# Performance work log

Measured on AMD Instinct MI355X. Metric: run time of the kernel, lower is better.

## Reference

```python
import jax, jax.numpy as jnp
import numpy as np

DIM = 512
HEADS = 16
HEAD_DIM = DIM // HEADS
SCALE = HEAD_DIM ** -0.5


def setup_inputs() -> dict:
    key = jax.random.key(0)
    k = jax.random.split(key, 6)
    B_, N = 2048, 49
    nW = 64
    x = jax.random.normal(k[0], (B_, N, DIM), dtype=jnp.float32)
    mask = jax.random.normal(k[1], (nW, N, N), dtype=jnp.float32)
    W_qkv = jax.random.normal(k[2], (3 * DIM, DIM), dtype=jnp.float32) * 0.02
    b_qkv = jnp.zeros((3 * DIM,), dtype=jnp.float32)
    W_proj = jax.random.normal(k[3], (DIM, DIM), dtype=jnp.float32) * 0.02
    b_proj = jnp.zeros((DIM,), dtype=jnp.float32)
    return {"x": x, "mask": mask, "W_qkv": W_qkv, "b_qkv": b_qkv,
            "W_proj": W_proj, "b_proj": b_proj}


def reference(x, mask, W_qkv, b_qkv, W_proj, b_proj):
    B_, N, C = x.shape
    H, d = HEADS, HEAD_DIM
    nW = mask.shape[0]
    # qkv projection: [B_, N, 3, H, d] -> q,k,v each [B_, H, N, d]
    qkv = (x @ W_qkv.T + b_qkv).reshape(B_, N, 3, H, d)
    qkv = jnp.transpose(qkv, (2, 0, 3, 1, 4))
    q, k, v = qkv[0], qkv[1], qkv[2]
    attn = jnp.einsum('bhnd,bhmd->bhnm', q * SCALE, k)  # [B_, H, N, N]
    # add per-window additive mask, broadcast over B_//nW groups and heads
    attn = attn.reshape(B_ // nW, nW, H, N, N) + mask[None, :, None, :, :]
    attn = attn.reshape(B_, H, N, N)
    attn = jax.nn.softmax(attn, axis=-1)
    out = jnp.einsum('bhnm,bhmd->bhnd', attn, v)  # [B_, H, N, d]
    out = jnp.transpose(out, (0, 2, 1, 3)).reshape(B_, N, C)
    return out @ W_proj.T + b_proj
```

## Files before the change

kernel.cpp:

```cpp
#include <hip/hip_runtime.h>


typedef unsigned short ushort_t;
typedef __bf16 bf16x8 __attribute__((ext_vector_type(8)));
typedef float f32x4 __attribute__((ext_vector_type(4)));
typedef unsigned short us8 __attribute__((ext_vector_type(8)));

#define SCALE_F 0.17677669529663687f

__device__ __forceinline__ ushort_t f2bf(float f) {
  unsigned u = __builtin_bit_cast(unsigned, f);
  u += 0x7FFFu + ((u >> 16) & 1u);
  return (ushort_t)(u >> 16);
}

__device__ __forceinline__ void gload_lds16(const void* g, void* l) {
  __builtin_amdgcn_global_load_lds(
      (const __attribute__((address_space(1))) void*)g,
      (__attribute__((address_space(3))) void*)l, 16, 0, 0);
}

__global__ __launch_bounds__(256) void k_cvt(const float* __restrict__ in,
                                             ushort_t* __restrict__ out, int n4) {
  int i = blockIdx.x * blockDim.x + threadIdx.x;
  if (i >= n4) return;
  float4 v = reinterpret_cast<const float4*>(in)[i];
  ushort4 o = make_ushort4(f2bf(v.x), f2bf(v.y), f2bf(v.z), f2bf(v.w));
  reinterpret_cast<ushort4*>(out)[i] = o;
}

__global__ __launch_bounds__(256) void k_gemm1f(const float* __restrict__ X,
                                                const ushort_t* __restrict__ W,
                                                const float* __restrict__ bias,
                                                ushort_t* __restrict__ out_qkv) {
  __shared__ __align__(16) float    Asf[128][64];
  __shared__ __align__(16) ushort_t Ws[128][64];
  constexpr int nt_o = 12;

  const int tid  = threadIdx.x;
  const int lane = tid & 63;
  const int wv   = tid >> 6;
  const int wr   = wv >> 1, wc = wv & 1;

  const int cpx = gridDim.x >> 3;
  const int lid = (blockIdx.x & 7) * cpx + (blockIdx.x >> 3);
  const int bm  = lid / nt_o;
  const int bo  = lid - bm * nt_o;
  const size_t m0 = (size_t)bm * 128;
  const int o0    = bo * 128;

  f32x4 acc[4][4];
#pragma unroll
  for (int i = 0; i < 4; i++)
#pragma unroll
    for (int j = 0; j < 4; j++) acc[i][j] = f32x4{0.f, 0.f, 0.f, 0.f};

  const int l15 = lane & 15;
  const int lq  = lane >> 4;
  int schA[4];
#pragma unroll
  for (int i = 0; i < 4; i++)
    schA[i] = (l15 ^ ((i * 4 + lq) & 15)) * 4;

  const int srowW = wv * 32 + (lane >> 3);
  const int schW  = ((lane & 7) ^ (lane >> 3)) * 8;
  const ushort_t* Wg = W + (size_t)(o0 + srowW) * 512 + schW;

  for (int kt = 0; kt < 8; ++kt) {
    const int k0 = kt * 64;
#pragma unroll
    for (int i = 0; i < 8; i++) {
      const float* g = X + (m0 + wv * 32 + i * 4 + lq) * 512 + k0 + schA[i & 3];
      gload_lds16(g, &Asf[wv * 32 + i * 4][0]);
    }
#pragma unroll
    for (int i = 0; i < 4; i++)
      gload_lds16(Wg + (size_t)i * (8 * 512) + k0, &Ws[wv * 32 + i * 8][0]);
    __syncthreads();

    const int fr = lane & 15;
#pragma unroll
    for (int kk = 0; kk < 2; ++kk) {
      const int cbW = (((kk * 4 + lq) ^ (lane & 7)) << 3);
      uint4 br[4];
#pragma unroll
      for (int ni = 0; ni < 4; ni++)
        br[ni] = *reinterpret_cast<const uint4*>(&Ws[wc * 64 + ni * 16 + fr][cbW]);
      bf16x8 ar[4];
      const int L0 = kk * 8 + lq * 2;
      const int s0 = (L0 ^ fr) * 4;
      const int s1 = ((L0 + 1) ^ fr) * 4;
#pragma unroll
      for (int mi = 0; mi < 4; mi++) {
        const float4 fa = *reinterpret_cast<const float4*>(&Asf[wr * 64 + mi * 16 + fr][s0]);
        const float4 fb = *reinterpret_cast<const float4*>(&Asf[wr * 64 + mi * 16 + fr][s1]);
        bf16x8 t;
        t[0] = (__bf16)fa.x; t[1] = (__bf16)fa.y; t[2] = (__bf16)fa.z; t[3] = (__bf16)fa.w;
        t[4] = (__bf16)fb.x; t[5] = (__bf16)fb.y; t[6] = (__bf16)fb.z; t[7] = (__bf16)fb.w;
        ar[mi] = t;
      }
#pragma unroll
      for (int mi = 0; mi < 4; mi++)
#pragma unroll
        for (int ni = 0; ni < 4; ni++)
          acc[mi][ni] = __builtin_amdgcn_mfma_f32_16x16x32_bf16(
              ar[mi], __builtin_bit_cast(bf16x8, br[ni]), acc[mi][ni], 0, 0, 0);
    }
    __syncthreads();
  }

  const int colbase = lane & 15;
  const int rowgrp  = (lane >> 4) * 4;
#pragma unroll
  for (int mi = 0; mi < 4; mi++) {
#pragma unroll
    for (int r = 0; r < 4; r++) {
      const size_t t = m0 + wr * 64 + mi * 16 + rowgrp + r;
      ushort_t* rowp = out_qkv + t * 1536;
#pragma unroll
      for (int ni = 0; ni < 4; ni++) {
        const int o = o0 + wc * 64 + ni * 16 + colbase;
        rowp[o] = f2bf(acc[mi][ni][r] + bias[o]);
      }
    }
  }
}

__global__ __launch_bounds__(256) void k_gemmB(const ushort_t* __restrict__ A,
                                               const ushort_t* __restrict__ W,
                                               const float* __restrict__ bias,
                                               float* __restrict__ out_f,
                                               int nt_o) {
  __shared__ __align__(16) ushort_t As[128][64];
  __shared__ __align__(16) ushort_t Ws[128][64];

  const int tid  = threadIdx.x;
  const int lane = tid & 63;
  const int wv   = tid >> 6;
  const int wr   = wv >> 1, wc = wv & 1;

  const int cpx = gridDim.x >> 3;
  const int lid = (blockIdx.x & 7) * cpx + (blockIdx.x >> 3);
  const int bm  = lid / nt_o;
  const int bo  = lid - bm * nt_o;
  const size_t m0 = (size_t)bm * 128;
  const int o0    = bo * 128;

  f32x4 acc[4][4];
#pragma unroll
  for (int i = 0; i < 4; i++)
#pragma unroll
    for (int j = 0; j < 4; j++) acc[i][j] = f32x4{0.f, 0.f, 0.f, 0.f};

  const int srow   = wv * 32 + (lane >> 3);
  const int schunk = (((lane & 7) ^ (lane >> 3)) * 8);

  for (int kt = 0; kt < 8; ++kt) {
    const int k0 = kt * 64;
#pragma unroll
    for (int i = 0; i < 4; i++)
      gload_lds16(A + (m0 + srow + i * 8) * 512 + k0 + schunk,
                  &As[wv * 32 + i * 8][0]);
#pragma unroll
    for (int i = 0; i < 4; i++)
      gload_lds16(W + (size_t)(o0 + srow + i * 8) * 512 + k0 + schunk,
                  &Ws[wv * 32 + i * 8][0]);
    __syncthreads();
    const int fr = lane & 15;
#pragma unroll
    for (int kk = 0; kk < 2; ++kk) {
      const int ch = kk * 4 + (lane >> 4);
      const int cb = ((ch ^ (lane & 7)) << 3);
      uint4 ar[4], br[4];
#pragma unroll
      for (int mi = 0; mi < 4; mi++)
        ar[mi] = *reinterpret_cast<const uint4*>(&As[wr * 64 + mi * 16 + fr][cb]);
#pragma unroll
      for (int ni = 0; ni < 4; ni++)
        br[ni] = *reinterpret_cast<const uint4*>(&Ws[wc * 64 + ni * 16 + fr][cb]);
#pragma unroll
      for (int mi = 0; mi < 4; mi++)
#pragma unroll
        for (int ni = 0; ni < 4; ni++)
          acc[mi][ni] = __builtin_amdgcn_mfma_f32_16x16x32_bf16(
              __builtin_bit_cast(bf16x8, ar[mi]),
              __builtin_bit_cast(bf16x8, br[ni]), acc[mi][ni], 0, 0, 0);
    }
    __syncthreads();
  }

  const int colbase = lane & 15;
  const int rowgrp  = (lane >> 4) * 4;
#pragma unroll
  for (int ni = 0; ni < 4; ni++) {
    const int o = o0 + wc * 64 + ni * 16 + colbase;
    const float bv = bias[o];
#pragma unroll
    for (int mi = 0; mi < 4; mi++) {
      const size_t mrow = m0 + wr * 64 + mi * 16 + rowgrp;
#pragma unroll
      for (int r = 0; r < 4; r++)
        out_f[(mrow + r) * 512 + o] = acc[mi][ni][r] + bv;
    }
  }
}

__global__ __launch_bounds__(256) void k_attn4(const ushort_t* __restrict__ qkv,
                                               const float* __restrict__ mask,
                                               ushort_t* __restrict__ aout) {
  __shared__ __align__(16) ushort_t Vt[4][32][64];
  __shared__ __align__(16) ushort_t Ps[4][64][64];

  const int tid  = threadIdx.x;
  const int lane = tid & 63;
  const int wv   = tid >> 6;
  const int blk  = blockIdx.x;
  const int b    = blk >> 2;
  const int h    = (blk & 3) * 4 + wv;
  const int w    = b & 63;
  const size_t tb = (size_t)b * 49 * 1536 + (size_t)h * 32;
  const ushort_t* qb = qkv + tb;
  const ushort_t* kb = qkv + tb + 512;
  const ushort_t* vb = qkv + tb + 1024;

  {
    uint4* vz = reinterpret_cast<uint4*>(&Vt[wv][0][0]);
#pragma unroll
    for (int i = 0; i < 4; i++) vz[i * 64 + lane] = make_uint4(0, 0, 0, 0);
  }
  __syncthreads();
#pragma unroll
  for (int i = 0; i < 4; i++) {
    const int e = lane + (i << 6);
    if (e < 196) {
      const int n = e >> 2, d0 = (e & 3) * 8;
      uint4 raw = *reinterpret_cast<const uint4*>(vb + (size_t)n * 1536 + d0);
      us8 ev = __builtin_bit_cast(us8, raw);
#pragma unroll
      for (int j = 0; j < 8; j++)
        Vt[wv][d0 + j][(((n >> 3) ^ j) << 3) | (n & 7)] = ev[j];
    }
  }

  const int arow = lane & 15;
  const int kc   = (lane >> 4) * 8;
  const int rg   = (lane >> 4) * 4;

  uint4 kf[4];
#pragma unroll
  for (int ni = 0; ni < 4; ni++)
    kf[ni] = *reinterpret_cast<const uint4*>(kb + (size_t)(ni * 16 + arow) * 1536 + kc);

  float rsum[4][4];

#pragma unroll
  for (int hm = 0; hm < 2; hm++) {
    f32x4 s2[2][4];
#pragma unroll
    for (int j = 0; j < 2; j++) {
      const int mt = hm * 2 + j;
      uint4 qraw = *reinterpret_cast<const uint4*>(qb + (size_t)(mt * 16 + arow) * 1536 + kc);
      bf16x8 qa = __builtin_bit_cast(bf16x8, qraw);
#pragma unroll
      for (int ni = 0; ni < 4; ni++) {
        f32x4 z = {0.f, 0.f, 0.f, 0.f};
        s2[j][ni] = __builtin_amdgcn_mfma_f32_16x16x32_bf16(
            qa, __builtin_bit_cast(bf16x8, kf[ni]), z, 0, 0, 0);
      }
    }
#pragma unroll
    for (int j = 0; j < 2; j++) {
      const int mt = hm * 2 + j;
#pragma unroll
      for (int r = 0; r < 4; r++) {
        const int qr = mt * 16 + rg + r;
        float sv[4];
        float mx = -1e30f;
#pragma unroll
        for (int ni = 0; ni < 4; ni++) {
          const int col = ni * 16 + arow;
          float v;
          if (qr < 49 && col < 49)
            v = s2[j][ni][r] * SCALE_F + mask[(size_t)w * 2401 + qr * 49 + col];
          else
            v = -1e30f;
          sv[ni] = v;
          mx = fmaxf(mx, v);
        }
#pragma unroll
        for (int off = 1; off < 16; off <<= 1) mx = fmaxf(mx, __shfl_xor(mx, off));
        float sum = 0.f;
        const int prow = rg + r;
#pragma unroll
        for (int ni = 0; ni < 4; ni++) {
          float p = __expf(sv[ni] - mx);
          sum += p;
          const int pcol = ni * 16 + arow;
          Ps[wv][mt * 16 + prow]
            [(((pcol >> 3) ^ (prow & 7)) << 3) | (pcol & 7)] = f2bf(p);
        }
#pragma unroll
        for (int off = 1; off < 16; off <<= 1) sum += __shfl_xor(sum, off);
        rsum[mt][r] = sum;
      }
    }
  }

  __syncthreads();

  uint4 vf0[2], vf1[2];
#pragma unroll
  for (int kk = 0; kk < 2; kk++) {
    const int ch = kk * 4 + (lane >> 4);
    const int cb = ((ch ^ (lane & 7)) << 3);
    vf0[kk] = *reinterpret_cast<const uint4*>(&Vt[wv][arow][cb]);
    vf1[kk] = *reinterpret_cast<const uint4*>(&Vt[wv][16 + arow][cb]);
  }

#pragma unroll
  for (int mt = 0; mt < 4; mt++) {
    f32x4 o0 = {0.f, 0.f, 0.f, 0.f}, o1 = {0.f, 0.f, 0.f, 0.f};
#pragma unroll
    for (int kk = 0; kk < 2; kk++) {
      const int ch = kk * 4 + (lane >> 4);
      const int cb = ((ch ^ (lane & 7)) << 3);
      uint4 praw = *reinterpret_cast<const uint4*>(&Ps[wv][mt * 16 + arow][cb]);
      bf16x8 pa = __builtin_bit_cast(bf16x8, praw);
      o0 = __builtin_amdgcn_mfma_f32_16x16x32_bf16(
          pa, __builtin_bit_cast(bf16x8, vf0[kk]), o0, 0, 0, 0);
      o1 = __builtin_amdgcn_mfma_f32_16x16x32_bf16(
          pa, __builtin_bit_cast(bf16x8, vf1[kk]), o1, 0, 0, 0);
    }
#pragma unroll
    for (int r = 0; r < 4; r++) {
      const int qr = mt * 16 + rg + r;
      if (qr < 49) {
        const float inv = 1.f / rsum[mt][r];
        aout[((size_t)b * 49 + qr) * 512 + h * 32 + arow]      = f2bf(o0[r] * inv);
        aout[((size_t)b * 49 + qr) * 512 + h * 32 + 16 + arow] = f2bf(o1[r] * inv);
      }
    }
  }
}

extern "C" void kernel_launch(void* const* d_in, const int* in_sizes, int n_in,
                              void* d_out, int out_size, void* d_ws, size_t ws_size,
                              hipStream_t stream) {
  const float* x      = (const float*)d_in[0];
  const float* mask   = (const float*)d_in[1];
  const float* W_qkv  = (const float*)d_in[2];
  const float* b_qkv  = (const float*)d_in[3];
  const float* W_proj = (const float*)d_in[4];
  const float* b_proj = (const float*)d_in[5];
  float* out = (float*)d_out;

  ushort_t* ws     = (ushort_t*)d_ws;
  ushort_t* qkvb   = ws;
  ushort_t* aoutb  = ws + 154140672UL;
  ushort_t* wqkvb  = ws + 205520896UL;
  ushort_t* wprojb = ws + 206307328UL;

  const int n4q = 786432 / 4, n4p = 262144 / 4;
  k_cvt<<<(n4q + 255) / 256, 256, 0, stream>>>(W_qkv, wqkvb, n4q);
  k_cvt<<<(n4p + 255) / 256, 256, 0, stream>>>(W_proj, wprojb, n4p);

  k_gemm1f<<<784 * 12, 256, 0, stream>>>(x, wqkvb, b_qkv, qkvb);

  k_attn4<<<2048 * 4, 256, 0, stream>>>(qkvb, mask, aoutb);

  k_gemmB<<<784 * 4, 256, 0, stream>>>(aoutb, wprojb, b_proj, out, 4);
}
```

Measured before the change: 599.7 us.

## Pre-convert x to bf16 and drop softmax max/sum reductions via MFMA row sums

The QKV GEMM now reads x from a separately converted bf16 copy instead of loading fp32 tiles and converting them inside the inner loop. This adds a standalone conversion pass over x, which costs an extra read of fp32 and a write plus re-read of bf16, but it halves the GEMM's A-tile LDS traffic. In attention, the per-row max subtraction and the shuffle-based sum reduction are removed: exponentials are taken directly and the row sums come from an extra MFMA against a ones vector. Skipping max subtraction risks overflow for large logits, and the bf16-rounded probabilities are what get summed.

```diff
diff --git a/kernel.cpp b/kernel.cpp
--- a/kernel.cpp
+++ b/kernel.cpp
@@ -29,11 +29,11 @@
   reinterpret_cast<ushort4*>(out)[i] = o;
 }
 
-__global__ __launch_bounds__(256) void k_gemm1f(const float* __restrict__ X,
-                                                const ushort_t* __restrict__ W,
-                                                const float* __restrict__ bias,
-                                                ushort_t* __restrict__ out_qkv) {
-  __shared__ __align__(16) float    Asf[128][64];
+__global__ __launch_bounds__(256) void k_gemm1(const ushort_t* __restrict__ A,
+                                               const ushort_t* __restrict__ W,
+                                               const float* __restrict__ bias,
+                                               ushort_t* __restrict__ out_qkv) {
+  __shared__ __align__(16) ushort_t As[128][64];
   __shared__ __align__(16) ushort_t Ws[128][64];
   constexpr int nt_o = 12;
 
@@ -55,56 +55,39 @@
 #pragma unroll
     for (int j = 0; j < 4; j++) acc[i][j] = f32x4{0.f, 0.f, 0.f, 0.f};
 
-  const int l15 = lane & 15;
-  const int lq  = lane >> 4;
-  int schA[4];
-#pragma unroll
-  for (int i = 0; i < 4; i++)
-    schA[i] = (l15 ^ ((i * 4 + lq) & 15)) * 4;
-
-  const int srowW = wv * 32 + (lane >> 3);
-  const int schW  = ((lane & 7) ^ (lane >> 3)) * 8;
-  const ushort_t* Wg = W + (size_t)(o0 + srowW) * 512 + schW;
+  const int srow   = wv * 32 + (lane >> 3);
+  const int schunk = (((lane & 7) ^ (lane >> 3)) * 8);
 
   for (int kt = 0; kt < 8; ++kt) {
     const int k0 = kt * 64;
 #pragma unroll
-    for (int i = 0; i < 8; i++) {
-      const float* g = X + (m0 + wv * 32 + i * 4 + lq) * 512 + k0 + schA[i & 3];
-      gload_lds16(g, &Asf[wv * 32 + i * 4][0]);
-    }
-#pragma unroll
     for (int i = 0; i < 4; i++)
-      gload_lds16(Wg + (size_t)i * (8 * 512) + k0, &Ws[wv * 32 + i * 8][0]);
+      gload_lds16(A + (m0 + srow + i * 8) * 512 + k0 + schunk,
+                  &As[wv * 32 + i * 8][0]);
+#pragma unroll
+    for (int i = 0; i < 4; i++)
+      gload_lds16(W + (size_t)(o0 + srow + i * 8) * 512 + k0 + schunk,
+                  &Ws[wv * 32 + i * 8][0]);
     __syncthreads();
-
     const int fr = lane & 15;
 #pragma unroll
     for (int kk = 0; kk < 2; ++kk) {
-      const int cbW = (((kk * 4 + lq) ^ (lane & 7)) << 3);
-      uint4 br[4];
+      const int ch = kk * 4 + (lane >> 4);
+      const int cb = ((ch ^ (lane & 7)) << 3);
+      uint4 ar[4], br[4];
+#pragma unroll
+      for (int mi = 0; mi < 4; mi++)
+        ar[mi] = *reinterpret_cast<const uint4*>(&As[wr * 64 + mi * 16 + fr][cb]);
 #pragma unroll
       for (int ni = 0; ni < 4; ni++)
-        br[ni] = *reinterpret_cast<const uint4*>(&Ws[wc * 64 + ni * 16 + fr][cbW]);
-      bf16x8 ar[4];
-      const int L0 = kk * 8 + lq * 2;
-      const int s0 = (L0 ^ fr) * 4;
-      const int s1 = ((L0 + 1) ^ fr) * 4;
-#pragma unroll
-      for (int mi = 0; mi < 4; mi++) {
-        const float4 fa = *reinterpret_cast<const float4*>(&Asf[wr * 64 + mi * 16 + fr][s0]);
-        const float4 fb = *reinterpret_cast<const float4*>(&Asf[wr * 64 + mi * 16 + fr][s1]);
-        bf16x8 t;
-        t[0] = (__bf16)fa.x; t[1] = (__bf16)fa.y; t[2] = (__bf16)fa.z; t[3] = (__bf16)fa.w;
-        t[4] = (__bf16)fb.x; t[5] = (__bf16)fb.y; t[6] = (__bf16)fb.z; t[7] = (__bf16)fb.w;
-        ar[mi] = t;
-      }
+        br[ni] = *reinterpret_cast<const uint4*>(&Ws[wc * 64 + ni * 16 + fr][cb]);
 #pragma unroll
       for (int mi = 0; mi < 4; mi++)
 #pragma unroll
         for (int ni = 0; ni < 4; ni++)
           acc[mi][ni] = __builtin_amdgcn_mfma_f32_16x16x32_bf16(
-              ar[mi], __builtin_bit_cast(bf16x8, br[ni]), acc[mi][ni], 0, 0, 0);
+              __builtin_bit_cast(bf16x8, ar[mi]),
+              __builtin_bit_cast(bf16x8, br[ni]), acc[mi][ni], 0, 0, 0);
     }
     __syncthreads();
   }
@@ -251,8 +234,6 @@
   for (int ni = 0; ni < 4; ni++)
     kf[ni] = *reinterpret_cast<const uint4*>(kb + (size_t)(ni * 16 + arow) * 1536 + kc);
 
-  float rsum[4][4];
-
 #pragma unroll
   for (int hm = 0; hm < 2; hm++) {
     f32x4 s2[2][4];
@@ -274,34 +255,19 @@
 #pragma unroll
       for (int r = 0; r < 4; r++) {
         const int qr = mt * 16 + rg + r;
-        float sv[4];
-        float mx = -1e30f;
+        const int prow = rg + r;
 #pragma unroll
         for (int ni = 0; ni < 4; ni++) {
           const int col = ni * 16 + arow;
-          float v;
+          float p;
           if (qr < 49 && col < 49)
-            v = s2[j][ni][r] * SCALE_F + mask[(size_t)w * 2401 + qr * 49 + col];
+            p = __expf(s2[j][ni][r] * SCALE_F + mask[(size_t)w * 2401 + qr * 49 + col]);
           else
-            v = -1e30f;
-          sv[ni] = v;
-          mx = fmaxf(mx, v);
-        }
-#pragma unroll
-        for (int off = 1; off < 16; off <<= 1) mx = fmaxf(mx, __shfl_xor(mx, off));
-        float sum = 0.f;
-        const int prow = rg + r;
-#pragma unroll
-        for (int ni = 0; ni < 4; ni++) {
-          float p = __expf(sv[ni] - mx);
-          sum += p;
+            p = 0.f;
           const int pcol = ni * 16 + arow;
           Ps[wv][mt * 16 + prow]
             [(((pcol >> 3) ^ (prow & 7)) << 3) | (pcol & 7)] = f2bf(p);
         }
-#pragma unroll
-        for (int off = 1; off < 16; off <<= 1) sum += __shfl_xor(sum, off);
-        rsum[mt][r] = sum;
       }
     }
   }
@@ -317,9 +283,14 @@
     vf1[kk] = *reinterpret_cast<const uint4*>(&Vt[wv][16 + arow][cb]);
   }
 
+  bf16x8 ones;
+#pragma unroll
+  for (int i = 0; i < 8; i++) ones[i] = (__bf16)1.0f;
+
 #pragma unroll
   for (int mt = 0; mt < 4; mt++) {
     f32x4 o0 = {0.f, 0.f, 0.f, 0.f}, o1 = {0.f, 0.f, 0.f, 0.f};
+    f32x4 o2 = {0.f, 0.f, 0.f, 0.f};
 #pragma unroll
     for (int kk = 0; kk < 2; kk++) {
       const int ch = kk * 4 + (lane >> 4);
@@ -330,12 +301,13 @@
           pa, __builtin_bit_cast(bf16x8, vf0[kk]), o0, 0, 0, 0);
       o1 = __builtin_amdgcn_mfma_f32_16x16x32_bf16(
           pa, __builtin_bit_cast(bf16x8, vf1[kk]), o1, 0, 0, 0);
+      o2 = __builtin_amdgcn_mfma_f32_16x16x32_bf16(pa, ones, o2, 0, 0, 0);
     }
 #pragma unroll
     for (int r = 0; r < 4; r++) {
       const int qr = mt * 16 + rg + r;
       if (qr < 49) {
-        const float inv = 1.f / rsum[mt][r];
+        const float inv = 1.f / o2[r];
         aout[((size_t)b * 49 + qr) * 512 + h * 32 + arow]      = f2bf(o0[r] * inv);
         aout[((size_t)b * 49 + qr) * 512 + h * 32 + 16 + arow] = f2bf(o1[r] * inv);
       }
@@ -355,16 +327,18 @@
   float* out = (float*)d_out;
 
   ushort_t* ws     = (ushort_t*)d_ws;
-  ushort_t* qkvb   = ws;
-  ushort_t* aoutb  = ws + 154140672UL;
-  ushort_t* wqkvb  = ws + 205520896UL;
-  ushort_t* wprojb = ws + 206307328UL;
-
-  const int n4q = 786432 / 4, n4p = 262144 / 4;
+  ushort_t* xb     = ws;
+  ushort_t* qkvb   = ws + 51380224UL;
+  ushort_t* aoutb  = ws + 205520896UL;
+  ushort_t* wqkvb  = ws + 256901120UL;
+  ushort_t* wprojb = ws + 257687552UL;
+
+  const int n4x = 51380224 / 4, n4q = 786432 / 4, n4p = 262144 / 4;
+  k_cvt<<<(n4x + 255) / 256, 256, 0, stream>>>(x, xb, n4x);
   k_cvt<<<(n4q + 255) / 256, 256, 0, stream>>>(W_qkv, wqkvb, n4q);
   k_cvt<<<(n4p + 255) / 256, 256, 0, stream>>>(W_proj, wprojb, n4p);
 
-  k_gemm1f<<<784 * 12, 256, 0, stream>>>(x, wqkvb, b_qkv, qkvb);
+  k_gemm1<<<784 * 12, 256, 0, stream>>>(xb, wqkvb, b_qkv, qkvb);
 
   k_attn4<<<2048 * 4, 256, 0, stream>>>(qkvb, mask, aoutb);
 
```

Measured after the change: 573.1 us. 1.05x faster.
